# Performance work log

Hardware: AMD Instinct MI355X
Metric: run time of the kernel (lower is better)

The kernel has to match this reference:

```python
import jax, jax.numpy as jnp
import numpy as np

N, E, F, D, EH, G, L, NG = 50000, 800000, 32, 32, 96, 128, 3, 500


def setup_inputs() -> dict:
    key = jax.random.key(0)
    ks = iter(jax.random.split(key, 32))
    w = lambda shape: jax.random.normal(next(ks), shape, dtype=jnp.float32) * 0.05
    inp = {
        "node_features": jax.random.normal(next(ks), (N, F), dtype=jnp.float32),
        "enc_W": w((F, D)), "enc_b": w((D,)),
        "msg_W1": w((L, 2 * D, EH)), "msg_b1": w((L, EH)),
        "msg_W2": w((L, EH, EH)), "msg_b2": w((L, EH)),
        "rmsg_W1": w((L, 2 * D, EH)), "rmsg_b1": w((L, EH)),
        "rmsg_W2": w((L, EH, EH)), "rmsg_b2": w((L, EH)),
        "gru_Wih": w((L, 3 * D, EH)), "gru_Whh": w((L, 3 * D, D)),
        "gru_bih": w((L, 3 * D)), "gru_bhh": w((L, 3 * D)),
        "agg_W1": w((D, 2 * G)), "agg_b1": w((2 * G,)),
        "agg_W2": w((G, G)), "agg_b2": w((G,)),
        "from_idx": jax.random.randint(next(ks), (E,), 0, N),
        "to_idx": jax.random.randint(next(ks), (E,), 0, N),
        "graph_idx": jnp.sort(jax.random.randint(next(ks), (N,), 0, NG)),
        "n_graphs": NG,
    }
    return inp


def _mlp(x, W1, b1, W2, b2):
    # Linear -> ReLU -> Linear (message net)
    return jax.nn.relu(x @ W1 + b1) @ W2 + b2


def _gru_step(x, h, Wih, Whh, bih, bhh):
    # torch nn.GRU single-step, gate order r, z, n
    gi = x @ Wih.T + bih  # [n, 3D]
    gh = h @ Whh.T + bhh  # [n, 3D]
    ir, iz, inn = jnp.split(gi, 3, axis=-1)
    hr, hz, hn = jnp.split(gh, 3, axis=-1)
    r = jax.nn.sigmoid(ir + hr)
    z = jax.nn.sigmoid(iz + hz)
    n = jnp.tanh(inn + r * hn)
    return (1.0 - z) * n + z * h


def _forward(node_features, enc_W, enc_b, msg_W1, msg_b1, msg_W2, msg_b2,
             rmsg_W1, rmsg_b1, rmsg_W2, rmsg_b2, gru_Wih, gru_Whh, gru_bih, gru_bhh,
             agg_W1, agg_b1, agg_W2, agg_b2, from_idx, to_idx, graph_idx, n_graphs):
    # GraphEncoder: single Linear
    h = node_features @ enc_W + enc_b  # [N, D]
    n_nodes = h.shape[0]
    n_layers = msg_W1.shape[0]
    for l in range(n_layers):  # small fixed layer count
        fs = h[from_idx]  # [E, D] gather
        ts = h[to_idx]    # [E, D] gather
        # forward-direction messages: gather -> concat -> MLP -> scatter_add to to_idx
        m = _mlp(jnp.concatenate([fs, ts], axis=-1), msg_W1[l], msg_b1[l], msg_W2[l], msg_b2[l])
        agg = jax.ops.segment_sum(m, to_idx, num_segments=n_nodes)
        # reverse direction: roles of from/to swapped, scatter to from_idx
        mr = _mlp(jnp.concatenate([ts, fs], axis=-1), rmsg_W1[l], rmsg_b1[l], rmsg_W2[l], rmsg_b2[l])
        agg = agg + jax.ops.segment_sum(mr, from_idx, num_segments=n_nodes)
        # node update via GRU (aggregated messages as input, node states as hidden)
        h = _gru_step(agg, h, gru_Wih[l], gru_Whh[l], gru_bih[l], gru_bhh[l])
    # GraphAggregator: gated node transform + scatter_add by graph, then Linear
    g = h @ agg_W1 + agg_b1  # [N, 2G]
    gdim = agg_W2.shape[0]
    gated = jax.nn.sigmoid(g[:, :gdim]) * g[:, gdim:]
    graph_states = jax.ops.segment_sum(gated, graph_idx, num_segments=n_graphs)  # [n_graphs, G]
    return graph_states @ agg_W2 + agg_b2


def reference(node_features, enc_W, enc_b, msg_W1, msg_b1, msg_W2, msg_b2,
              rmsg_W1, rmsg_b1, rmsg_W2, rmsg_b2, gru_Wih, gru_Whh, gru_bih, gru_bhh,
              agg_W1, agg_b1, agg_W2, agg_b2, from_idx, to_idx, graph_idx, n_graphs):
    return _forward(node_features, enc_W, enc_b, msg_W1, msg_b1, msg_W2, msg_b2,
                    rmsg_W1, rmsg_b1, rmsg_W2, rmsg_b2, gru_Wih, gru_Whh, gru_bih, gru_bhh,
                    agg_W1, agg_b1, agg_W2, agg_b2, from_idx, to_idx, graph_idx, n_graphs)
```

## Files before the change

### kernel.cpp

```cpp
#include <hip/hip_runtime.h>

#define SB 512

typedef __attribute__((ext_vector_type(8))) short short8;
typedef __attribute__((ext_vector_type(4))) float f32x4;

__device__ inline unsigned short f2bf(float f) {
    unsigned u = __float_as_uint(f);
    unsigned r = (u + 0x7fffu + ((u >> 16) & 1u)) >> 16;
    return (unsigned short)r;
}
__device__ inline unsigned pack2bf(float x, float y) {
    return (unsigned)f2bf(x) | ((unsigned)f2bf(y) << 16);
}

__global__ void count_rank_kernel(const int* __restrict__ from_idx, const int* __restrict__ to_idx,
                                  int* __restrict__ cnt_to, int* __restrict__ cnt_from,
                                  int* __restrict__ rank_to, int* __restrict__ rank_from, int E) {
    int e = blockIdx.x * blockDim.x + threadIdx.x;
    if (e >= E) return;
    int f = from_idx[e], t = to_idx[e];
    rank_to[e] = atomicAdd(&cnt_to[t], 1);
    rank_from[e] = atomicAdd(&cnt_from[f], 1);
}

__global__ void __launch_bounds__(SB) scanA_kernel(const int* __restrict__ cnt_to,
                                                   const int* __restrict__ cnt_from,
                                                   int* __restrict__ bsum, int nblk, int N) {
    const int* cnt = blockIdx.y ? cnt_from : cnt_to;
    __shared__ int s[SB];
    int tid = threadIdx.x;
    int i = blockIdx.x * SB + tid;
    s[tid] = (i < N) ? cnt[i] : 0;
    __syncthreads();
    for (int d = SB / 2; d > 0; d >>= 1) {
        if (tid < d) s[tid] += s[tid + d];
        __syncthreads();
    }
    if (tid == 0) bsum[blockIdx.y * nblk + blockIdx.x] = s[0];
}

__global__ void scanB_kernel(int* __restrict__ bsum, int* __restrict__ bbase,
                             int* __restrict__ off_to, int* __restrict__ off_from,
                             int nblk, int N) {
    int tid = threadIdx.x;
    if (tid < 2) {
        const int* bs = bsum + tid * nblk;
        int* bb = bbase + tid * nblk;
        int run = 0;
        for (int i = 0; i < nblk; ++i) { bb[i] = run; run += bs[i]; }
        if (tid == 0) off_to[N] = run; else off_from[N] = run;
    }
}

__global__ void __launch_bounds__(SB) scanC_kernel(const int* __restrict__ cnt_to,
                                                   const int* __restrict__ cnt_from,
                                                   const int* __restrict__ bbase,
                                                   int* __restrict__ off_to, int* __restrict__ off_from,
                                                   int nblk, int N) {
    const int* cnt = blockIdx.y ? cnt_from : cnt_to;
    int* off = blockIdx.y ? off_from : off_to;
    __shared__ int s[SB];
    int tid = threadIdx.x;
    int i = blockIdx.x * SB + tid;
    int v = (i < N) ? cnt[i] : 0;
    s[tid] = v;
    __syncthreads();
    for (int d = 1; d < SB; d <<= 1) {
        int t = s[tid];
        int add = (tid >= d) ? s[tid - d] : 0;
        __syncthreads();
        s[tid] = t + add;
        __syncthreads();
    }
    if (i < N) off[i] = s[tid] - v + bbase[blockIdx.y * nblk + blockIdx.x];
}

__global__ void fill_kernel(const int* __restrict__ from_idx, const int* __restrict__ to_idx,
                            const int* __restrict__ off_to, const int* __restrict__ off_from,
                            const int* __restrict__ rank_to, const int* __restrict__ rank_from,
                            int* __restrict__ list_to, int* __restrict__ list_from, int E) {
    int e = blockIdx.x * blockDim.x + threadIdx.x;
    if (e >= E) return;
    int f = from_idx[e], t = to_idx[e];
    list_to[off_to[t] + rank_to[e]] = f;
    list_from[off_from[f] + rank_from[e]] = t;
}

__global__ void compose_kernel(const float* __restrict__ W2, const float* __restrict__ rW2,
                               const float* __restrict__ Wih,
                               const float* __restrict__ b2, const float* __restrict__ rb2,
                               float* __restrict__ M1, float* __restrict__ M2,
                               float* __restrict__ v12) {
    int l = blockIdx.x / 97, j = blockIdx.x % 97;
    int k = threadIdx.x;
    const float* wih = Wih + l * 9216 + k * 96;
    if (j < 96) {
        const float* w2  = W2 + l * 9216 + j * 96;
        const float* rw2 = rW2 + l * 9216 + j * 96;
        float a1 = 0.f, a2 = 0.f;
        for (int m = 0; m < 96; ++m) {
            float wv = wih[m];
            a1 = fmaf(w2[m], wv, a1);
            a2 = fmaf(rw2[m], wv, a2);
        }
        M1[l * 9216 + j * 96 + k] = a1;
        M2[l * 9216 + j * 96 + k] = a2;
    } else {
        const float* bb = b2 + l * 96;
        const float* rbb = rb2 + l * 96;
        float a1 = 0.f, a2 = 0.f;
        for (int m = 0; m < 96; ++m) {
            float wv = wih[m];
            a1 = fmaf(bb[m], wv, a1);
            a2 = fmaf(rbb[m], wv, a2);
        }
        v12[l * 192 + k] = a1;
        v12[l * 192 + 96 + k] = a2;
    }
}

__global__ void repack_kernel(const float* __restrict__ M1, const float* __restrict__ M2,
                              const float* __restrict__ Whh,
                              const float* __restrict__ W1f, const float* __restrict__ W1r,
                              unsigned* __restrict__ M1bc, unsigned* __restrict__ M2bc,
                              unsigned* __restrict__ Whhbc, unsigned* __restrict__ W1bc) {
    int idx = blockIdx.x * 256 + threadIdx.x;
    if (idx < 13824) {
        int l = idx / 4608, r = idx % 4608, c = r / 48, wd = r % 48;
        const float* src = M1 + l * 9216;
        M1bc[idx] = pack2bf(src[(2 * wd) * 96 + c], src[(2 * wd + 1) * 96 + c]);
    } else if (idx < 27648) {
        int j = idx - 13824;
        int l = j / 4608, r = j % 4608, c = r / 48, wd = r % 48;
        const float* src = M2 + l * 9216;
        M2bc[j] = pack2bf(src[(2 * wd) * 96 + c], src[(2 * wd + 1) * 96 + c]);
    } else if (idx < 32256) {
        int j = idx - 27648;
        int l = j / 1536, r = j % 1536, c = r / 16, wd = r % 16;
        const float* src = Whh + l * 3072 + c * 32;
        Whhbc[j] = pack2bf(src[2 * wd], src[2 * wd + 1]);
    } else if (idx < 32256 + 18432) {
        int j = idx - 32256;
        int l = j / 6144, r = j % 6144, C = r / 16, wd = r % 16;
        const float* src; int col, rb;
        if (C < 96)       { src = W1f + l * 6144; col = C;       rb = 0;  }
        else if (C < 192) { src = W1f + l * 6144; col = C - 96;  rb = 32; }
        else if (C < 288) { src = W1r + l * 6144; col = C - 192; rb = 0;  }
        else              { src = W1r + l * 6144; col = C - 288; rb = 32; }
        W1bc[j] = pack2bf(src[(rb + 2 * wd) * 96 + col], src[(rb + 2 * wd + 1) * 96 + col]);
    }
}

__global__ void __launch_bounds__(256) enc_gemm(const float* __restrict__ IN,
                                                const float* __restrict__ W, const float* __restrict__ bias,
                                                float* __restrict__ OUT, unsigned short* __restrict__ hb16, int N) {
    __shared__ float tile[64][33];
    int n0 = blockIdx.x * 64, tid = threadIdx.x;
    for (int idx = tid; idx < 64 * 32; idx += 256) {
        int r = idx >> 5, c = idx & 31;
        int n = n0 + r;
        tile[r][c] = (n < N) ? IN[(long)n * 32 + c] : 0.f;
    }
    __syncthreads();
    int lane = tid & 63;
    int w = __builtin_amdgcn_readfirstlane(tid >> 6);
    float acc[8] = {0};
    const float* Wp = W + w * 8;
#pragma unroll 4
    for (int j = 0; j < 32; ++j) {
        float a = tile[lane][j];
#pragma unroll
        for (int c = 0; c < 8; ++c) acc[c] = fmaf(a, Wp[j * 32 + c], acc[c]);
    }
    int n = n0 + lane;
    if (n >= N) return;
    float* outp = OUT + (long)n * 32 + w * 8;
    unsigned short* bp = hb16 + (long)n * 32 + w * 8;
#pragma unroll
    for (int c = 0; c < 8; ++c) {
        float v = acc[c] + bias[w * 8 + c];
        outp[c] = v;
        bp[c] = f2bf(v);
    }
}

__global__ void __launch_bounds__(512) proj_mfma(
    const unsigned* __restrict__ hb, const unsigned* __restrict__ W1bc,
    const float* __restrict__ b1f, const float* __restrict__ b1r,
    unsigned short* __restrict__ PaF16, unsigned short* __restrict__ PbF16,
    unsigned short* __restrict__ PaR16, unsigned short* __restrict__ PbR16, int N)
{
    int tid = threadIdx.x;
    int lane = tid & 63;
    int w = __builtin_amdgcn_readfirstlane(tid >> 6);
    int nt = w >> 1, cg = w & 1;
    int kgrp = lane >> 4, l15 = lane & 15;
    int ntile = blockIdx.x * 64 + nt * 16;
    int arow = ntile + l15;
    long arc = (arow < N) ? arow : (N - 1);
    short8 a = *(const short8*)(hb + arc * 16 + kgrp * 4);

    unsigned short* Pa16 = cg ? PaR16 : PaF16;
    unsigned short* Pb16 = cg ? PbR16 : PbF16;
    const float* b1 = cg ? b1r : b1f;

    f32x4 acc[12];
#pragma unroll
    for (int ct = 0; ct < 12; ++ct) {
        int col = cg * 192 + ct * 16 + l15;
        short8 b = *(const short8*)(W1bc + (long)col * 16 + kgrp * 4);
        acc[ct] = __builtin_amdgcn_mfma_f32_16x16x32_bf16(a, b, (f32x4){0.f,0.f,0.f,0.f}, 0, 0, 0);
    }
    int nbase = ntile + kgrp * 4;
#pragma unroll
    for (int ct = 0; ct < 6; ++ct) {
        int col = ct * 16 + l15;
#pragma unroll
        for (int i = 0; i < 4; ++i) {
            int n = nbase + i;
            if (n < N) Pa16[(long)n * 96 + col] = f2bf(acc[ct][i]);
        }
    }
#pragma unroll
    for (int ct = 6; ct < 12; ++ct) {
        int col = (ct - 6) * 16 + l15;
        float bv = b1[col];
#pragma unroll
        for (int i = 0; i < 4; ++i) {
            int n = nbase + i;
            if (n < N) Pb16[(long)n * 96 + col] = f2bf(acc[ct][i] + bv);
        }
    }
}

__global__ void __launch_bounds__(256) agg_bf16(
    const int* __restrict__ offF, const int* __restrict__ listF,
    const int* __restrict__ offR, const int* __restrict__ listR,
    const unsigned* __restrict__ PaF, const unsigned* __restrict__ PaR,
    const unsigned short* __restrict__ PbF16, const unsigned short* __restrict__ PbR16,
    unsigned* __restrict__ AFb, unsigned* __restrict__ ARb, int N)
{
    const int* off; const int* list; const unsigned* Pa; const unsigned short* Pb16; unsigned* AB;
    if (blockIdx.y == 0) { off = offF; list = listF; Pa = PaF; Pb16 = PbF16; AB = AFb; }
    else                 { off = offR; list = listR; Pa = PaR; Pb16 = PbR16; AB = ARb; }
    int n = __builtin_amdgcn_readfirstlane((blockIdx.x * 256 + threadIdx.x) >> 6);
    int lane = threadIdx.x & 63;
    if (n >= N) return;
    int li = (lane < 48) ? lane : 47;
    bool act = lane < 48;
    float sx = 0.f, sy = 0.f;
    if (act) {
        unsigned s = *(const unsigned*)(Pb16 + (long)n * 96 + 2 * li);
        sx = __uint_as_float(s << 16);
        sy = __uint_as_float(s & 0xffff0000u);
    }
    float a0 = 0.f, a1 = 0.f;
    int beg = off[n], end = off[n + 1];
    if (end > beg) {
        int nb = (end - beg + 7) >> 3;
        for (int b = 0; b < nb; ++b) {
            int base = beg + b * 8;
            unsigned u[8]; float m[8];
#pragma unroll
            for (int q = 0; q < 8; ++q) {
                int idx = base + q;
                bool v = idx < end;
                int src = list[v ? idx : end - 1];
                u[q] = Pa[(long)src * 48 + li];
                m[q] = v ? 1.f : 0.f;
            }
#pragma unroll
            for (int q = 0; q < 8; ++q) {
                a0 += m[q] * fmaxf(__uint_as_float(u[q] << 16) + sx, 0.f);
                a1 += m[q] * fmaxf(__uint_as_float(u[q] & 0xffff0000u) + sy, 0.f);
            }
        }
    }
    if (act) AB[(long)n * 48 + li] = pack2bf(a0, a1);
}

template <int DO_PROJ>
__global__ void __launch_bounds__(512) gru3_proj(
    const unsigned* __restrict__ AFb, const unsigned* __restrict__ ARb,
    const unsigned* __restrict__ M1bc, const unsigned* __restrict__ M2bc,
    const unsigned* __restrict__ Whhbc,
    const float* __restrict__ v12,
    const int* __restrict__ offF, const int* __restrict__ offR,
    const float* __restrict__ h, const unsigned* __restrict__ hb,
    const float* __restrict__ bih, const float* __restrict__ bhh,
    float* __restrict__ hout, unsigned short* __restrict__ hbout,
    const unsigned* __restrict__ W1bc, const float* __restrict__ b1f, const float* __restrict__ b1r,
    unsigned short* __restrict__ PaF16, unsigned short* __restrict__ PbF16,
    unsigned short* __restrict__ PaR16, unsigned short* __restrict__ PbR16, int N)
{
    __shared__ unsigned short hs[64 * 40];
    int tid = threadIdx.x;
    int lane = tid & 63;
    int w = __builtin_amdgcn_readfirstlane(tid >> 6);
    int nt = w >> 1, cg = w & 1;
    int kgrp = lane >> 4, l15 = lane & 15;
    int c = cg * 16 + l15;
    int ntile = blockIdx.x * 64 + nt * 16;
    int arow = ntile + l15;
    long arc = (arow < N) ? arow : (N - 1);

    f32x4 acc[3]; f32x4 gh[3];
#pragma unroll
    for (int g = 0; g < 3; ++g) { acc[g] = (f32x4){0.f,0.f,0.f,0.f}; gh[g] = (f32x4){0.f,0.f,0.f,0.f}; }

    const unsigned* afp = AFb + arc * 48 + kgrp * 4;
    const unsigned* arp = ARb + arc * 48 + kgrp * 4;
#pragma unroll
    for (int k0 = 0; k0 < 3; ++k0) {
        short8 a = *(const short8*)(afp + k0 * 16);
#pragma unroll
        for (int g = 0; g < 3; ++g) {
            int col = g * 32 + c;
            short8 b = *(const short8*)(M1bc + (long)col * 48 + k0 * 16 + kgrp * 4);
            acc[g] = __builtin_amdgcn_mfma_f32_16x16x32_bf16(a, b, acc[g], 0, 0, 0);
        }
    }
#pragma unroll
    for (int k0 = 0; k0 < 3; ++k0) {
        short8 a = *(const short8*)(arp + k0 * 16);
#pragma unroll
        for (int g = 0; g < 3; ++g) {
            int col = g * 32 + c;
            short8 b = *(const short8*)(M2bc + (long)col * 48 + k0 * 16 + kgrp * 4);
            acc[g] = __builtin_amdgcn_mfma_f32_16x16x32_bf16(a, b, acc[g], 0, 0, 0);
        }
    }
    {
        short8 ha = *(const short8*)(hb + arc * 16 + kgrp * 4);
#pragma unroll
        for (int g = 0; g < 3; ++g) {
            int col = g * 32 + c;
            short8 b = *(const short8*)(Whhbc + (long)col * 16 + kgrp * 4);
            gh[g] = __builtin_amdgcn_mfma_f32_16x16x32_bf16(ha, b, gh[g], 0, 0, 0);
        }
    }

    float v1r[3], v2r[3], bihv[3], bhhv[3];
#pragma unroll
    for (int g = 0; g < 3; ++g) {
        int col = g * 32 + c;
        v1r[g] = v12[col]; v2r[g] = v12[96 + col];
        bihv[g] = bih[col]; bhhv[g] = bhh[col];
    }
    int nbase = ntile + kgrp * 4;
#pragma unroll
    for (int i = 0; i < 4; ++i) {
        int n = nbase + i;
        if (n < N) {
            float dF = (float)(offF[n + 1] - offF[n]);
            float dR = (float)(offR[n + 1] - offR[n]);
            float gir = acc[0][i] + dF * v1r[0] + dR * v2r[0] + bihv[0];
            float giz = acc[1][i] + dF * v1r[1] + dR * v2r[1] + bihv[1];
            float gin = acc[2][i] + dF * v1r[2] + dR * v2r[2] + bihv[2];
            float r = 1.f / (1.f + __expf(-(gir + gh[0][i] + bhhv[0])));
            float z = 1.f / (1.f + __expf(-(giz + gh[1][i] + bhhv[1])));
            float nn = tanhf(gin + r * (gh[2][i] + bhhv[2]));
            float hv = h[(long)n * 32 + c];
            float vout = (1.f - z) * nn + z * hv;
            hout[(long)n * 32 + c] = vout;
            unsigned short v16 = f2bf(vout);
            hbout[(long)n * 32 + c] = v16;
            if (DO_PROJ) hs[(nt * 16 + kgrp * 4 + i) * 40 + c] = v16;
        }
    }
    if (DO_PROJ) {
        __syncthreads();
        const unsigned* hsw = (const unsigned*)hs;
        short8 a = *(const short8*)(hsw + (nt * 16 + l15) * 20 + kgrp * 4);
        unsigned short* Pa16 = cg ? PaR16 : PaF16;
        unsigned short* Pb16 = cg ? PbR16 : PbF16;
        const float* b1 = cg ? b1r : b1f;
        f32x4 pacc[12];
#pragma unroll
        for (int ct = 0; ct < 12; ++ct) {
            int col = cg * 192 + ct * 16 + l15;
            short8 b = *(const short8*)(W1bc + (long)col * 16 + kgrp * 4);
            pacc[ct] = __builtin_amdgcn_mfma_f32_16x16x32_bf16(a, b, (f32x4){0.f,0.f,0.f,0.f}, 0, 0, 0);
        }
#pragma unroll
        for (int ct = 0; ct < 6; ++ct) {
            int col = ct * 16 + l15;
#pragma unroll
            for (int i = 0; i < 4; ++i) {
                int n = nbase + i;
                if (n < N) Pa16[(long)n * 96 + col] = f2bf(pacc[ct][i]);
            }
        }
#pragma unroll
        for (int ct = 6; ct < 12; ++ct) {
            int col = (ct - 6) * 16 + l15;
            float bv = b1[col];
#pragma unroll
            for (int i = 0; i < 4; ++i) {
                int n = nbase + i;
                if (n < N) Pb16[(long)n * 96 + col] = f2bf(pacc[ct][i] + bv);
            }
        }
    }
}

__global__ void __launch_bounds__(128) graph_agg(const float* __restrict__ h, const float* __restrict__ W1,
                          const float* __restrict__ b1, const int* __restrict__ gidx,
                          float* __restrict__ gs, int N, int chunk) {
    int k = threadIdx.x;
    int n_start = blockIdx.x * chunk;
    if (n_start >= N) return;
    int n_end = min(n_start + chunk, N);
    float w1[32], w2[32];
#pragma unroll
    for (int j = 0; j < 32; ++j) {
        w1[j] = W1[j * 256 + k];
        w2[j] = W1[j * 256 + 128 + k];
    }
    float bb1 = b1[k], bb2 = b1[128 + k];
    float acc = 0.f;
    int cur = gidx[n_start];
    for (int n = n_start; n < n_end; ++n) {
        int g = gidx[n];
        if (g != cur) { atomicAdd(&gs[cur * 128 + k], acc); acc = 0.f; cur = g; }
        float g1 = bb1, g2 = bb2;
#pragma unroll
        for (int j = 0; j < 32; ++j) {
            float hv = h[(long)n * 32 + j];
            g1 = fmaf(hv, w1[j], g1);
            g2 = fmaf(hv, w2[j], g2);
        }
        acc += (1.f / (1.f + __expf(-g1))) * g2;
    }
    atomicAdd(&gs[cur * 128 + k], acc);
}

__global__ void final_gemm(const float* __restrict__ gs, const float* __restrict__ W,
                           const float* __restrict__ b, float* __restrict__ out) {
    int g = blockIdx.x, k = threadIdx.x;
    float a = b[k];
#pragma unroll 8
    for (int j = 0; j < 128; ++j) a = fmaf(gs[g * 128 + j], W[j * 128 + k], a);
    out[g * 128 + k] = a;
}

extern "C" void kernel_launch(void* const* d_in, const int* in_sizes, int n_in,
                              void* d_out, int out_size, void* d_ws, size_t ws_size,
                              hipStream_t stream) {
    const float* node_features = (const float*)d_in[0];
    const float* enc_W  = (const float*)d_in[1];
    const float* enc_b  = (const float*)d_in[2];
    const float* msg_W1 = (const float*)d_in[3];
    const float* msg_b1 = (const float*)d_in[4];
    const float* msg_W2 = (const float*)d_in[5];
    const float* msg_b2 = (const float*)d_in[6];
    const float* rmsg_W1 = (const float*)d_in[7];
    const float* rmsg_b1 = (const float*)d_in[8];
    const float* rmsg_W2 = (const float*)d_in[9];
    const float* rmsg_b2 = (const float*)d_in[10];
    const float* gru_Wih = (const float*)d_in[11];
    const float* gru_Whh = (const float*)d_in[12];
    const float* gru_bih = (const float*)d_in[13];
    const float* gru_bhh = (const float*)d_in[14];
    const float* agg_W1 = (const float*)d_in[15];
    const float* agg_b1 = (const float*)d_in[16];
    const float* agg_W2 = (const float*)d_in[17];
    const float* agg_b2 = (const float*)d_in[18];
    const int* from_idx = (const int*)d_in[19];
    const int* to_idx   = (const int*)d_in[20];
    const int* graph_idx = (const int*)d_in[21];

    const int N = in_sizes[0] / 32;
    const int E = in_sizes[19];
    const int NG = out_size / 128;
    float* out = (float*)d_out;

    char* ws = (char*)d_ws;
    auto alloc = [&](size_t b) { void* p = (void*)ws; ws += (b + 255) & ~(size_t)255; return p; };
    int* cnt2     = (int*)alloc((size_t)2 * N * 4);
    int* cnt_to   = cnt2;
    int* cnt_from = cnt2 + N;
    int* off_to   = (int*)alloc((size_t)(N + 1) * 4);
    int* off_from = (int*)alloc((size_t)(N + 1) * 4);
    int* list_to  = (int*)alloc((size_t)E * 4);
    int* list_from= (int*)alloc((size_t)E * 4);
    float* h0  = (float*)alloc((size_t)N * 32 * 4);
    float* h1  = (float*)alloc((size_t)N * 32 * 4);
    unsigned* PaF = (unsigned*)alloc((size_t)N * 48 * 4);
    unsigned* PaR = (unsigned*)alloc((size_t)N * 48 * 4);
    unsigned short* PbF16 = (unsigned short*)alloc((size_t)N * 96 * 2);
    unsigned short* PbR16 = (unsigned short*)alloc((size_t)N * 96 * 2);
    unsigned* AFb = (unsigned*)alloc((size_t)N * 48 * 4);
    unsigned* ARb = (unsigned*)alloc((size_t)N * 48 * 4);
    unsigned* hb0 = (unsigned*)alloc((size_t)N * 16 * 4);
    unsigned* hb1 = (unsigned*)alloc((size_t)N * 16 * 4);
    float* M1   = (float*)alloc((size_t)3 * 96 * 96 * 4);
    float* M2   = (float*)alloc((size_t)3 * 96 * 96 * 4);
    float* v12  = (float*)alloc((size_t)3 * 192 * 4);
    unsigned* M1bc = (unsigned*)alloc((size_t)13824 * 4);
    unsigned* M2bc = (unsigned*)alloc((size_t)13824 * 4);
    unsigned* Whhbc = (unsigned*)alloc((size_t)4608 * 4);
    unsigned* W1bc  = (unsigned*)alloc((size_t)18432 * 4);
    float* gs   = (float*)alloc((size_t)NG * 128 * 4);
    const int nblk = (N + SB - 1) / SB;
    int* bsum  = (int*)alloc((size_t)2 * nblk * 4);
    int* bbase = (int*)alloc((size_t)2 * nblk * 4);
    int* rank_to   = (int*)PaF;
    int* rank_from = (int*)PaR;

    hipMemsetAsync(cnt2, 0, (size_t)2 * N * 4, stream);
    hipMemsetAsync(gs, 0, (size_t)NG * 128 * 4, stream);

    int gE = (E + 255) / 256;
    count_rank_kernel<<<gE, 256, 0, stream>>>(from_idx, to_idx, cnt_to, cnt_from, rank_to, rank_from, E);
    dim3 gScan(nblk, 2);
    scanA_kernel<<<gScan, SB, 0, stream>>>(cnt_to, cnt_from, bsum, nblk, N);
    scanB_kernel<<<1, 64, 0, stream>>>(bsum, bbase, off_to, off_from, nblk, N);
    scanC_kernel<<<gScan, SB, 0, stream>>>(cnt_to, cnt_from, bbase, off_to, off_from, nblk, N);
    fill_kernel<<<gE, 256, 0, stream>>>(from_idx, to_idx, off_to, off_from, rank_to, rank_from,
                                        list_to, list_from, E);

    compose_kernel<<<3 * 97, 96, 0, stream>>>(msg_W2, rmsg_W2, gru_Wih, msg_b2, rmsg_b2, M1, M2, v12);
    repack_kernel<<<(32256 + 18432 + 255) / 256, 256, 0, stream>>>(M1, M2, gru_Whh, msg_W1, rmsg_W1,
                                                                   M1bc, M2bc, Whhbc, W1bc);

    int gN64 = (N + 63) / 64;
    enc_gemm<<<gN64, 256, 0, stream>>>(node_features, enc_W, enc_b, h0, (unsigned short*)hb0, N);

    proj_mfma<<<gN64, 512, 0, stream>>>(hb0, W1bc,
                                        msg_b1, rmsg_b1,
                                        (unsigned short*)PaF, PbF16, (unsigned short*)PaR, PbR16, N);

    float* hcur = h0; float* hnext = h1;
    unsigned* hbcur = hb0; unsigned* hbnext = hb1;
    dim3 gAgg((N + 3) / 4, 2);
    for (int l = 0; l < 3; ++l) {
        agg_bf16<<<gAgg, 256, 0, stream>>>(off_to, list_to, off_from, list_from,
                                           PaF, PaR, PbF16, PbR16, AFb, ARb, N);
        if (l < 2) {
            gru3_proj<1><<<gN64, 512, 0, stream>>>(AFb, ARb, M1bc + l * 4608, M2bc + l * 4608,
                                                   Whhbc + l * 1536, v12 + l * 192,
                                                   off_to, off_from, hcur, hbcur,
                                                   gru_bih + l * 96, gru_bhh + l * 96, hnext,
                                                   (unsigned short*)hbnext,
                                                   W1bc + (l + 1) * 6144, msg_b1 + (l + 1) * 96,
                                                   rmsg_b1 + (l + 1) * 96,
                                                   (unsigned short*)PaF, PbF16,
                                                   (unsigned short*)PaR, PbR16, N);
        } else {
            gru3_proj<0><<<gN64, 512, 0, stream>>>(AFb, ARb, M1bc + l * 4608, M2bc + l * 4608,
                                                   Whhbc + l * 1536, v12 + l * 192,
                                                   off_to, off_from, hcur, hbcur,
                                                   gru_bih + l * 96, gru_bhh + l * 96, hnext,
                                                   (unsigned short*)hbnext,
                                                   nullptr, nullptr, nullptr,
                                                   nullptr, nullptr, nullptr, nullptr, N);
        }
        float* t = hcur; hcur = hnext; hnext = t;
        unsigned* tb = hbcur; hbcur = hbnext; hbnext = tb;
    }

    const int chunk = 32;
    graph_agg<<<(N + chunk - 1) / chunk, 128, 0, stream>>>(hcur, agg_W1, agg_b1, graph_idx, gs, N, chunk);
    final_gemm<<<NG, 128, 0, stream>>>(gs, agg_W2, agg_b2, out);
}
```

Before: 427.6 us.

## Store adjacency lists as uint16 and keep node state only in bf16

Adjacency lists and per-edge ranks are narrowed from int32 to uint16, which halves the index traffic in the fill and aggregation kernels. The fp32 hidden state is dropped. The GRU now reads the previous hidden state from its bf16 copy, and fp32 output is written only in the final layer for the graph aggregator. This cuts memory traffic per layer but loses precision in the recurrent state update. It also relies on N fitting in 16 bits (50000 < 65536) and on per-node degree staying below 65536.

```diff
diff --git a/kernel.cpp b/kernel.cpp
--- a/kernel.cpp
+++ b/kernel.cpp
@@ -16,12 +16,13 @@
 
 __global__ void count_rank_kernel(const int* __restrict__ from_idx, const int* __restrict__ to_idx,
                                   int* __restrict__ cnt_to, int* __restrict__ cnt_from,
-                                  int* __restrict__ rank_to, int* __restrict__ rank_from, int E) {
+                                  unsigned short* __restrict__ rank_to,
+                                  unsigned short* __restrict__ rank_from, int E) {
     int e = blockIdx.x * blockDim.x + threadIdx.x;
     if (e >= E) return;
     int f = from_idx[e], t = to_idx[e];
-    rank_to[e] = atomicAdd(&cnt_to[t], 1);
-    rank_from[e] = atomicAdd(&cnt_from[f], 1);
+    rank_to[e] = (unsigned short)atomicAdd(&cnt_to[t], 1);
+    rank_from[e] = (unsigned short)atomicAdd(&cnt_from[f], 1);
 }
 
 __global__ void __launch_bounds__(SB) scanA_kernel(const int* __restrict__ cnt_to,
@@ -78,13 +79,15 @@
 
 __global__ void fill_kernel(const int* __restrict__ from_idx, const int* __restrict__ to_idx,
                             const int* __restrict__ off_to, const int* __restrict__ off_from,
-                            const int* __restrict__ rank_to, const int* __restrict__ rank_from,
-                            int* __restrict__ list_to, int* __restrict__ list_from, int E) {
+                            const unsigned short* __restrict__ rank_to,
+                            const unsigned short* __restrict__ rank_from,
+                            unsigned short* __restrict__ list_to,
+                            unsigned short* __restrict__ list_from, int E) {
     int e = blockIdx.x * blockDim.x + threadIdx.x;
     if (e >= E) return;
     int f = from_idx[e], t = to_idx[e];
-    list_to[off_to[t] + rank_to[e]] = f;
-    list_from[off_from[f] + rank_from[e]] = t;
+    list_to[off_to[t] + rank_to[e]] = (unsigned short)f;
+    list_from[off_from[f] + rank_from[e]] = (unsigned short)t;
 }
 
 __global__ void compose_kernel(const float* __restrict__ W2, const float* __restrict__ rW2,
@@ -154,7 +157,7 @@
 
 __global__ void __launch_bounds__(256) enc_gemm(const float* __restrict__ IN,
                                                 const float* __restrict__ W, const float* __restrict__ bias,
-                                                float* __restrict__ OUT, unsigned short* __restrict__ hb16, int N) {
+                                                unsigned short* __restrict__ hb16, int N) {
     __shared__ float tile[64][33];
     int n0 = blockIdx.x * 64, tid = threadIdx.x;
     for (int idx = tid; idx < 64 * 32; idx += 256) {
@@ -175,14 +178,9 @@
     }
     int n = n0 + lane;
     if (n >= N) return;
-    float* outp = OUT + (long)n * 32 + w * 8;
     unsigned short* bp = hb16 + (long)n * 32 + w * 8;
 #pragma unroll
-    for (int c = 0; c < 8; ++c) {
-        float v = acc[c] + bias[w * 8 + c];
-        outp[c] = v;
-        bp[c] = f2bf(v);
-    }
+    for (int c = 0; c < 8; ++c) bp[c] = f2bf(acc[c] + bias[w * 8 + c]);
 }
 
 __global__ void __launch_bounds__(512) proj_mfma(
@@ -235,13 +233,14 @@
 }
 
 __global__ void __launch_bounds__(256) agg_bf16(
-    const int* __restrict__ offF, const int* __restrict__ listF,
-    const int* __restrict__ offR, const int* __restrict__ listR,
+    const int* __restrict__ offF, const unsigned short* __restrict__ listF,
+    const int* __restrict__ offR, const unsigned short* __restrict__ listR,
     const unsigned* __restrict__ PaF, const unsigned* __restrict__ PaR,
     const unsigned short* __restrict__ PbF16, const unsigned short* __restrict__ PbR16,
     unsigned* __restrict__ AFb, unsigned* __restrict__ ARb, int N)
 {
-    const int* off; const int* list; const unsigned* Pa; const unsigned short* Pb16; unsigned* AB;
+    const int* off; const unsigned short* list; const unsigned* Pa;
+    const unsigned short* Pb16; unsigned* AB;
     if (blockIdx.y == 0) { off = offF; list = listF; Pa = PaF; Pb16 = PbF16; AB = AFb; }
     else                 { off = offR; list = listR; Pa = PaR; Pb16 = PbR16; AB = ARb; }
     int n = __builtin_amdgcn_readfirstlane((blockIdx.x * 256 + threadIdx.x) >> 6);
@@ -287,7 +286,7 @@
     const unsigned* __restrict__ Whhbc,
     const float* __restrict__ v12,
     const int* __restrict__ offF, const int* __restrict__ offR,
-    const float* __restrict__ h, const unsigned* __restrict__ hb,
+    const unsigned* __restrict__ hb,
     const float* __restrict__ bih, const float* __restrict__ bhh,
     float* __restrict__ hout, unsigned short* __restrict__ hbout,
     const unsigned* __restrict__ W1bc, const float* __restrict__ b1f, const float* __restrict__ b1r,
@@ -348,6 +347,7 @@
         v1r[g] = v12[col]; v2r[g] = v12[96 + col];
         bihv[g] = bih[col]; bhhv[g] = bhh[col];
     }
+    const unsigned short* hb16 = (const unsigned short*)hb;
     int nbase = ntile + kgrp * 4;
 #pragma unroll
     for (int i = 0; i < 4; ++i) {
@@ -361,12 +361,15 @@
             float r = 1.f / (1.f + __expf(-(gir + gh[0][i] + bhhv[0])));
             float z = 1.f / (1.f + __expf(-(giz + gh[1][i] + bhhv[1])));
             float nn = tanhf(gin + r * (gh[2][i] + bhhv[2]));
-            float hv = h[(long)n * 32 + c];
+            float hv = __uint_as_float((unsigned)hb16[(long)n * 32 + c] << 16);
             float vout = (1.f - z) * nn + z * hv;
-            hout[(long)n * 32 + c] = vout;
-            unsigned short v16 = f2bf(vout);
-            hbout[(long)n * 32 + c] = v16;
-            if (DO_PROJ) hs[(nt * 16 + kgrp * 4 + i) * 40 + c] = v16;
+            if (DO_PROJ) {
+                unsigned short v16 = f2bf(vout);
+                hbout[(long)n * 32 + c] = v16;
+                hs[(nt * 16 + kgrp * 4 + i) * 40 + c] = v16;
+            } else {
+                hout[(long)n * 32 + c] = vout;
+            }
         }
     }
     if (DO_PROJ) {
@@ -483,10 +486,9 @@
     int* cnt_from = cnt2 + N;
     int* off_to   = (int*)alloc((size_t)(N + 1) * 4);
     int* off_from = (int*)alloc((size_t)(N + 1) * 4);
-    int* list_to  = (int*)alloc((size_t)E * 4);
-    int* list_from= (int*)alloc((size_t)E * 4);
-    float* h0  = (float*)alloc((size_t)N * 32 * 4);
-    float* h1  = (float*)alloc((size_t)N * 32 * 4);
+    unsigned short* list_to  = (unsigned short*)alloc((size_t)E * 2);
+    unsigned short* list_from= (unsigned short*)alloc((size_t)E * 2);
+    float* hfin = (float*)alloc((size_t)N * 32 * 4);
     unsigned* PaF = (unsigned*)alloc((size_t)N * 48 * 4);
     unsigned* PaR = (unsigned*)alloc((size_t)N * 48 * 4);
     unsigned short* PbF16 = (unsigned short*)alloc((size_t)N * 96 * 2);
@@ -506,8 +508,8 @@
     const int nblk = (N + SB - 1) / SB;
     int* bsum  = (int*)alloc((size_t)2 * nblk * 4);
     int* bbase = (int*)alloc((size_t)2 * nblk * 4);
-    int* rank_to   = (int*)PaF;
-    int* rank_from = (int*)PaR;
+    unsigned short* rank_to   = (unsigned short*)PaF;
+    unsigned short* rank_from = (unsigned short*)PaR;
 
     hipMemsetAsync(cnt2, 0, (size_t)2 * N * 4, stream);
     hipMemsetAsync(gs, 0, (size_t)NG * 128 * 4, stream);
@@ -526,13 +528,11 @@
                                                                    M1bc, M2bc, Whhbc, W1bc);
 
     int gN64 = (N + 63) / 64;
-    enc_gemm<<<gN64, 256, 0, stream>>>(node_features, enc_W, enc_b, h0, (unsigned short*)hb0, N);
-
-    proj_mfma<<<gN64, 512, 0, stream>>>(hb0, W1bc,
-                                        msg_b1, rmsg_b1,
+    enc_gemm<<<gN64, 256, 0, stream>>>(node_features, enc_W, enc_b, (unsigned short*)hb0, N);
+
+    proj_mfma<<<gN64, 512, 0, stream>>>(hb0, W1bc, msg_b1, rmsg_b1,
                                         (unsigned short*)PaF, PbF16, (unsigned short*)PaR, PbR16, N);
 
-    float* hcur = h0; float* hnext = h1;
     unsigned* hbcur = hb0; unsigned* hbnext = hb1;
     dim3 gAgg((N + 3) / 4, 2);
     for (int l = 0; l < 3; ++l) {
@@ -541,9 +541,9 @@
         if (l < 2) {
             gru3_proj<1><<<gN64, 512, 0, stream>>>(AFb, ARb, M1bc + l * 4608, M2bc + l * 4608,
                                                    Whhbc + l * 1536, v12 + l * 192,
-                                                   off_to, off_from, hcur, hbcur,
-                                                   gru_bih + l * 96, gru_bhh + l * 96, hnext,
-                                                   (unsigned short*)hbnext,
+                                                   off_to, off_from, hbcur,
+                                                   gru_bih + l * 96, gru_bhh + l * 96,
+                                                   nullptr, (unsigned short*)hbnext,
                                                    W1bc + (l + 1) * 6144, msg_b1 + (l + 1) * 96,
                                                    rmsg_b1 + (l + 1) * 96,
                                                    (unsigned short*)PaF, PbF16,
@@ -551,17 +551,16 @@
         } else {
             gru3_proj<0><<<gN64, 512, 0, stream>>>(AFb, ARb, M1bc + l * 4608, M2bc + l * 4608,
                                                    Whhbc + l * 1536, v12 + l * 192,
-                                                   off_to, off_from, hcur, hbcur,
-                                                   gru_bih + l * 96, gru_bhh + l * 96, hnext,
-                                                   (unsigned short*)hbnext,
+                                                   off_to, off_from, hbcur,
+                                                   gru_bih + l * 96, gru_bhh + l * 96,
+                                                   hfin, nullptr,
                                                    nullptr, nullptr, nullptr,
                                                    nullptr, nullptr, nullptr, nullptr, N);
         }
-        float* t = hcur; hcur = hnext; hnext = t;
         unsigned* tb = hbcur; hbcur = hbnext; hbnext = tb;
     }
 
     const int chunk = 32;
-    graph_agg<<<(N + chunk - 1) / chunk, 128, 0, stream>>>(hcur, agg_W1, agg_b1, graph_idx, gs, N, chunk);
+    graph_agg<<<(N + chunk - 1) / chunk, 128, 0, stream>>>(hfin, agg_W1, agg_b1, graph_idx, gs, N, chunk);
     final_gemm<<<NG, 128, 0, stream>>>(gs, agg_W2, agg_b2, out);
 }
```

Result: no change. 420.1 us (-1.7%).
